# Kernel optimization log

Hardware: AMD Instinct MI355X
Metric: run time of the kernel (lower is better)

Reference implementation:

```python
import jax, jax.numpy as jnp
import numpy as np
from jax import lax

THRESHOLD = 0.3  # nn.Threshold(threshold, 0): y = x if x > threshold else 0
KERNEL = 3       # 3x3 maxpool, stride 1, pad 1 (SAME)


def setup_inputs() -> dict:
    key = jax.random.key(0)
    # [B=1, C=7, H, W] raw feature map (pre-sigmoid logits) from the UNet head
    feature = jax.random.normal(key, (1, 7, 2048, 2048), dtype=jnp.float32)
    return {"feature": feature, "max_detections": 4096}


def reference(feature, max_detections):
    # split along channel dim: 5 keypoint heatmaps, 1 side logit, 1 size logit
    heatmap = feature[:, :5]   # [1,5,H,W]
    side = feature[:, 5:6]     # [1,1,H,W]
    sizes = feature[:, 6:7]    # [1,1,H,W]

    activated = jax.nn.sigmoid(heatmap)
    thresholded = jnp.where(activated > THRESHOLD, activated, jnp.zeros((), activated.dtype))
    # 3x3 stride-1 SAME maxpool (local-max NMS)
    pooled = lax.reduce_window(thresholded, -jnp.inf, lax.max,
                               (1, 1, KERNEL, KERNEL), (1, 1, 1, 1), 'SAME')
    peak_mask = (pooled == thresholded)
    masked = (thresholded * peak_mask.astype(thresholded.dtype))[0]  # [5,H,W]
    masked_bool = masked > 0                                          # [5,H,W]

    side_act = jax.nn.sigmoid(side)[0, 0]    # [H,W]
    sizes_act = jax.nn.sigmoid(sizes)[0, 0]  # [H,W]
    probs_full = jnp.max(activated[0], axis=0)  # [H,W] max over 5 channels

    # fixed-size nonzero (jit-shapeable equivalent of torch .nonzero()/masked_select;
    # entries past the true count are padded with index 0 and zeroed out)
    c, y, x = jnp.nonzero(masked_bool, size=max_detections, fill_value=0)
    n_valid = jnp.sum(masked_bool)
    valid = (jnp.arange(max_detections) < n_valid).astype(probs_full.dtype)

    coords = jnp.stack([c, y, x], axis=1)           # [K,3] like torch nonzero order
    probs = probs_full[y, x] * valid                # masked_select broadcasts [H,W] vs [5,H,W]
    size_width = sizes_act[y, x] * valid
    size_height = sizes_act[y, x] * valid
    side_sel = side_act[y, x] * valid
    return probs, coords, size_width, size_height, side_sel
```

## Files before the change

kernel.cpp:

```cpp
#include <hip/hip_runtime.h>
#include <stdint.h>

#define IMG_H 2048
#define IMG_W 2048
#define CH_PIX (IMG_H * IMG_W)
#define ROWS_PER_BLOCK 8
#define MAXDET 4096
#define NBLK_A 1280
#define WORDS_PER_BLOCK 256

__device__ __forceinline__ float sigmoidf_(float v) {
    return 1.0f / (1.0f + expf(-v));
}

__device__ __forceinline__ float thr_load(const float* __restrict__ chan, int y, int x) {
    if ((unsigned)y >= (unsigned)IMG_H) return 0.0f;
    float a = sigmoidf_(chan[y * IMG_W + x]);
    return a > 0.3f ? a : 0.0f;
}

__global__ __launch_bounds__(256) void zero_out_k(float* __restrict__ out, int n) {
    int i = blockIdx.x * 256 + threadIdx.x;
    if (i < n) out[i] = 0.0f;
}

__global__ __launch_bounds__(256) void pass_a(const float* __restrict__ feat,
                                              uint64_t* __restrict__ masks,
                                              unsigned* __restrict__ counts) {
    int blk = blockIdx.x;
    int c = blk >> 8;
    int ytile = blk & 255;
    int y0 = ytile * ROWS_PER_BLOCK;
    const float* chan = feat + (size_t)c * CH_PIX;
    int t = threadIdx.x;
    int wave = t >> 6, lane = t & 63;

    __shared__ float colmax[IMG_W + 2];
    __shared__ unsigned wsum_lds[4];

    float thrprev[8], thrcur[8], thrnext[8];
#pragma unroll
    for (int j = 0; j < 8; ++j) {
        int x = j * 256 + t;
        thrprev[j] = thr_load(chan, y0 - 1, x);
        thrcur[j]  = thr_load(chan, y0,     x);
    }
    if (t == 0) { colmax[0] = 0.0f; colmax[IMG_W + 1] = 0.0f; }

    unsigned wcnt = 0;
    uint64_t base_widx = (uint64_t)blk * WORDS_PER_BLOCK;

    for (int r = 0; r < ROWS_PER_BLOCK; ++r) {
        int y = y0 + r;
#pragma unroll
        for (int j = 0; j < 8; ++j) {
            int x = j * 256 + t;
            thrnext[j] = thr_load(chan, y + 1, x);
            colmax[x + 1] = fmaxf(fmaxf(thrprev[j], thrcur[j]), thrnext[j]);
        }
        __syncthreads();
#pragma unroll
        for (int j = 0; j < 8; ++j) {
            int x = j * 256 + t;
            float pooled = fmaxf(fmaxf(colmax[x], colmax[x + 1]), colmax[x + 2]);
            bool pred = (thrcur[j] > 0.0f) && (pooled == thrcur[j]);
            uint64_t m = __ballot(pred);
            if (lane == 0) {
                masks[base_widx + (uint64_t)((r * 8 + j) * 4 + wave)] = m;
                wcnt += (unsigned)__popcll(m);
            }
        }
        __syncthreads();
#pragma unroll
        for (int j = 0; j < 8; ++j) { thrprev[j] = thrcur[j]; thrcur[j] = thrnext[j]; }
    }
    if (lane == 0) wsum_lds[wave] = wcnt;
    __syncthreads();
    if (t == 0) counts[blk] = wsum_lds[0] + wsum_lds[1] + wsum_lds[2] + wsum_lds[3];
}

__global__ __launch_bounds__(256) void scan_k(unsigned* __restrict__ data, int n) {
    __shared__ unsigned tmp[256];
    __shared__ unsigned carry;
    int t = threadIdx.x;
    if (t == 0) carry = 0;
    __syncthreads();
    for (int base = 0; base < n; base += 256) {
        unsigned v = (base + t < n) ? data[base + t] : 0u;
        tmp[t] = v;
        __syncthreads();
        for (int off = 1; off < 256; off <<= 1) {
            unsigned u = (t >= off) ? tmp[t - off] : 0u;
            __syncthreads();
            tmp[t] += u;
            __syncthreads();
        }
        unsigned incl = tmp[t];
        unsigned c0 = carry;
        __syncthreads();
        if (base + t < n) data[base + t] = c0 + incl - v;
        if (t == 255) carry = c0 + incl;
        __syncthreads();
    }
}

__global__ __launch_bounds__(256) void pass_c(const float* __restrict__ feat,
                                              const uint64_t* __restrict__ masks,
                                              const unsigned* __restrict__ offsets,
                                              float* __restrict__ out) {
    int blk = blockIdx.x;
    unsigned boff = offsets[blk];
    if (boff >= MAXDET) return;
    int t = threadIdx.x;
    uint64_t w = masks[(uint64_t)blk * WORDS_PER_BLOCK + t];
    unsigned cnt = (unsigned)__popcll(w);
    __shared__ unsigned tmp[256];
    tmp[t] = cnt;
    __syncthreads();
    for (int off = 1; off < 256; off <<= 1) {
        unsigned u = (t >= off) ? tmp[t - off] : 0u;
        __syncthreads();
        tmp[t] += u;
        __syncthreads();
    }
    unsigned rank = boff + tmp[t] - cnt;
    while (w) {
        int b = __ffsll((unsigned long long)w) - 1;
        w &= w - 1;
        if (rank < MAXDET) {
            uint64_t p = ((uint64_t)blk * WORDS_PER_BLOCK + (uint64_t)t) * 64ull + (uint64_t)b;
            int c = (int)(p / CH_PIX);
            int rem = (int)(p % CH_PIX);
            int y = rem >> 11, x = rem & 2047;
            size_t pix = (size_t)y * IMG_W + x;
            float pm = sigmoidf_(feat[pix]);
#pragma unroll
            for (int ch = 1; ch < 5; ++ch)
                pm = fmaxf(pm, sigmoidf_(feat[(size_t)ch * CH_PIX + pix]));
            float sdv = sigmoidf_(feat[(size_t)5 * CH_PIX + pix]);
            float szv = sigmoidf_(feat[(size_t)6 * CH_PIX + pix]);
            out[rank] = pm;
            out[MAXDET + rank * 3 + 0] = (float)c;
            out[MAXDET + rank * 3 + 1] = (float)y;
            out[MAXDET + rank * 3 + 2] = (float)x;
            out[16384 + rank] = szv;
            out[20480 + rank] = szv;
            out[24576 + rank] = sdv;
        }
        rank++;
    }
}

extern "C" void kernel_launch(void* const* d_in, const int* in_sizes, int n_in,
                              void* d_out, int out_size, void* d_ws, size_t ws_size,
                              hipStream_t stream) {
    const float* feat = (const float*)d_in[0];
    float* out = (float*)d_out;
    uint64_t* masks = (uint64_t*)d_ws;
    unsigned* counts = (unsigned*)((char*)d_ws + (size_t)NBLK_A * WORDS_PER_BLOCK * 8);

    zero_out_k<<<(out_size + 255) / 256, 256, 0, stream>>>(out, out_size);
    pass_a<<<NBLK_A, 256, 0, stream>>>(feat, masks, counts);
    scan_k<<<1, 256, 0, stream>>>(counts, NBLK_A);
    pass_c<<<NBLK_A, 256, 0, stream>>>(feat, masks, counts, out);
}
```

Before: 207.0 us.

## Use per-thread 8-pixel strips with byte masks and fold scan into compaction pass

Pass A now gives each thread 8 contiguous pixels loaded as float4s plus halo, computes the 3x3 max in registers, and writes one mask byte per thread per row. This removes the shared-memory colmax and block barriers and doubles rows per block. The separate zero-fill and single-block scan kernels are removed: each compaction block reduces all block counts itself, and the last block zero-fills the tail. Two launches replace four, at the cost of redundant count reductions in every block and halo loads repeated by neighbouring threads.

```diff
diff --git a/kernel.cpp b/kernel.cpp
--- a/kernel.cpp
+++ b/kernel.cpp
@@ -4,116 +4,153 @@
 #define IMG_H 2048
 #define IMG_W 2048
 #define CH_PIX (IMG_H * IMG_W)
-#define ROWS_PER_BLOCK 8
 #define MAXDET 4096
-#define NBLK_A 1280
-#define WORDS_PER_BLOCK 256
+#define NCH_HM 5
+#define ROWS_PER_BLOCK 16
+#define NBLK 640
+#define WPB 512
 
 __device__ __forceinline__ float sigmoidf_(float v) {
     return 1.0f / (1.0f + expf(-v));
 }
-
-__device__ __forceinline__ float thr_load(const float* __restrict__ chan, int y, int x) {
-    if ((unsigned)y >= (unsigned)IMG_H) return 0.0f;
-    float a = sigmoidf_(chan[y * IMG_W + x]);
+__device__ __forceinline__ float sigthr_(float v) {
+    float a = 1.0f / (1.0f + expf(-v));
     return a > 0.3f ? a : 0.0f;
 }
 
-__global__ __launch_bounds__(256) void zero_out_k(float* __restrict__ out, int n) {
-    int i = blockIdx.x * 256 + threadIdx.x;
-    if (i < n) out[i] = 0.0f;
+__device__ __forceinline__ void load_row(const float* __restrict__ chan, int y,
+                                         int xb, float* L) {
+    if ((unsigned)y >= (unsigned)IMG_H) {
+#pragma unroll
+        for (int k = 0; k < 10; ++k) L[k] = 0.0f;
+        return;
+    }
+    const float* row = chan + (size_t)y * IMG_W + xb;
+    float4 a = *(const float4*)(row);
+    float4 b = *(const float4*)(row + 4);
+    L[1] = sigthr_(a.x); L[2] = sigthr_(a.y); L[3] = sigthr_(a.z); L[4] = sigthr_(a.w);
+    L[5] = sigthr_(b.x); L[6] = sigthr_(b.y); L[7] = sigthr_(b.z); L[8] = sigthr_(b.w);
+    L[0] = (xb > 0)            ? sigthr_(row[-1]) : 0.0f;
+    L[9] = (xb + 8 < IMG_W)    ? sigthr_(row[8])  : 0.0f;
 }
 
 __global__ __launch_bounds__(256) void pass_a(const float* __restrict__ feat,
-                                              uint64_t* __restrict__ masks,
+                                              uint8_t* __restrict__ mask_bytes,
                                               unsigned* __restrict__ counts) {
     int blk = blockIdx.x;
-    int c = blk >> 8;
-    int ytile = blk & 255;
-    int y0 = ytile * ROWS_PER_BLOCK;
+    int c = blk >> 7;
+    int ytile = blk & 127;
+    int y0 = ytile << 4;
     const float* chan = feat + (size_t)c * CH_PIX;
     int t = threadIdx.x;
-    int wave = t >> 6, lane = t & 63;
+    int xb = t << 3;
 
-    __shared__ float colmax[IMG_W + 2];
-    __shared__ unsigned wsum_lds[4];
-
-    float thrprev[8], thrcur[8], thrnext[8];
-#pragma unroll
-    for (int j = 0; j < 8; ++j) {
-        int x = j * 256 + t;
-        thrprev[j] = thr_load(chan, y0 - 1, x);
-        thrcur[j]  = thr_load(chan, y0,     x);
-    }
-    if (t == 0) { colmax[0] = 0.0f; colmax[IMG_W + 1] = 0.0f; }
+    float tp[10], tc[10], tn[10];
+    load_row(chan, y0 - 1, xb, tp);
+    load_row(chan, y0,     xb, tc);
 
     unsigned wcnt = 0;
-    uint64_t base_widx = (uint64_t)blk * WORDS_PER_BLOCK;
+    size_t byte_base = (size_t)c * (CH_PIX / 8) + (size_t)y0 * (IMG_W / 8) + t;
 
     for (int r = 0; r < ROWS_PER_BLOCK; ++r) {
-        int y = y0 + r;
+        load_row(chan, y0 + r + 1, xb, tn);
+        float cm[10];
+#pragma unroll
+        for (int k = 0; k < 10; ++k) cm[k] = fmaxf(fmaxf(tp[k], tc[k]), tn[k]);
+        unsigned byte = 0;
 #pragma unroll
         for (int j = 0; j < 8; ++j) {
-            int x = j * 256 + t;
-            thrnext[j] = thr_load(chan, y + 1, x);
-            colmax[x + 1] = fmaxf(fmaxf(thrprev[j], thrcur[j]), thrnext[j]);
+            float own = tc[j + 1];
+            float pooled = fmaxf(fmaxf(cm[j], cm[j + 1]), cm[j + 2]);
+            if (own > 0.0f && pooled == own) byte |= (1u << j);
         }
-        __syncthreads();
+        mask_bytes[byte_base + (size_t)r * (IMG_W / 8)] = (uint8_t)byte;
+        wcnt += __popc(byte);
 #pragma unroll
-        for (int j = 0; j < 8; ++j) {
-            int x = j * 256 + t;
-            float pooled = fmaxf(fmaxf(colmax[x], colmax[x + 1]), colmax[x + 2]);
-            bool pred = (thrcur[j] > 0.0f) && (pooled == thrcur[j]);
-            uint64_t m = __ballot(pred);
-            if (lane == 0) {
-                masks[base_widx + (uint64_t)((r * 8 + j) * 4 + wave)] = m;
-                wcnt += (unsigned)__popcll(m);
-            }
-        }
-        __syncthreads();
+        for (int k = 0; k < 10; ++k) { tp[k] = tc[k]; tc[k] = tn[k]; }
+    }
+
 #pragma unroll
-        for (int j = 0; j < 8; ++j) { thrprev[j] = thrcur[j]; thrcur[j] = thrnext[j]; }
-    }
-    if (lane == 0) wsum_lds[wave] = wcnt;
+    for (int off = 32; off; off >>= 1) wcnt += __shfl_down(wcnt, off, 64);
+    __shared__ unsigned s[4];
+    int wave = t >> 6, lane = t & 63;
+    if (lane == 0) s[wave] = wcnt;
     __syncthreads();
-    if (t == 0) counts[blk] = wsum_lds[0] + wsum_lds[1] + wsum_lds[2] + wsum_lds[3];
+    if (t == 0) counts[blk] = s[0] + s[1] + s[2] + s[3];
 }
 
-__global__ __launch_bounds__(256) void scan_k(unsigned* __restrict__ data, int n) {
-    __shared__ unsigned tmp[256];
-    __shared__ unsigned carry;
-    int t = threadIdx.x;
-    if (t == 0) carry = 0;
-    __syncthreads();
-    for (int base = 0; base < n; base += 256) {
-        unsigned v = (base + t < n) ? data[base + t] : 0u;
-        tmp[t] = v;
-        __syncthreads();
-        for (int off = 1; off < 256; off <<= 1) {
-            unsigned u = (t >= off) ? tmp[t - off] : 0u;
-            __syncthreads();
-            tmp[t] += u;
-            __syncthreads();
+__device__ __forceinline__ void emit_word(uint64_t w, uint64_t pbase, unsigned& rank,
+                                          const float* __restrict__ feat,
+                                          float* __restrict__ out) {
+    while (w) {
+        int b = __ffsll((unsigned long long)w) - 1;
+        w &= w - 1;
+        if (rank < MAXDET) {
+            uint64_t p = pbase + (uint64_t)b;
+            int c = (int)(p >> 22);
+            int rem = (int)(p & (CH_PIX - 1));
+            int y = rem >> 11, x = rem & 2047;
+            size_t pix = (size_t)y * IMG_W + x;
+            float pm = sigmoidf_(feat[pix]);
+#pragma unroll
+            for (int ch = 1; ch < NCH_HM; ++ch)
+                pm = fmaxf(pm, sigmoidf_(feat[(size_t)ch * CH_PIX + pix]));
+            float sdv = sigmoidf_(feat[(size_t)5 * CH_PIX + pix]);
+            float szv = sigmoidf_(feat[(size_t)6 * CH_PIX + pix]);
+            out[rank] = pm;
+            out[MAXDET + rank * 3 + 0] = (float)c;
+            out[MAXDET + rank * 3 + 1] = (float)y;
+            out[MAXDET + rank * 3 + 2] = (float)x;
+            out[4 * MAXDET + rank] = szv;
+            out[5 * MAXDET + rank] = szv;
+            out[6 * MAXDET + rank] = sdv;
         }
-        unsigned incl = tmp[t];
-        unsigned c0 = carry;
-        __syncthreads();
-        if (base + t < n) data[base + t] = c0 + incl - v;
-        if (t == 255) carry = c0 + incl;
-        __syncthreads();
+        rank++;
     }
 }
 
 __global__ __launch_bounds__(256) void pass_c(const float* __restrict__ feat,
                                               const uint64_t* __restrict__ masks,
-                                              const unsigned* __restrict__ offsets,
+                                              const unsigned* __restrict__ counts,
                                               float* __restrict__ out) {
     int blk = blockIdx.x;
-    unsigned boff = offsets[blk];
+    int t = threadIdx.x;
+
+    unsigned p_lt = 0, p_all = 0;
+    for (int i = t; i < NBLK; i += 256) {
+        unsigned v = counts[i];
+        p_all += v;
+        if (i < blk) p_lt += v;
+    }
+#pragma unroll
+    for (int off = 32; off; off >>= 1) {
+        p_lt  += __shfl_down(p_lt,  off, 64);
+        p_all += __shfl_down(p_all, off, 64);
+    }
+    __shared__ unsigned sl[4], sa[4];
+    int wave = t >> 6, lane = t & 63;
+    if (lane == 0) { sl[wave] = p_lt; sa[wave] = p_all; }
+    __syncthreads();
+    unsigned boff  = sl[0] + sl[1] + sl[2] + sl[3];
+    unsigned total = sa[0] + sa[1] + sa[2] + sa[3];
+
+    if (blk == NBLK - 1) {
+        unsigned start = total < MAXDET ? total : MAXDET;
+        for (unsigned k = start + t; k < MAXDET; k += 256) {
+            out[k] = 0.0f;
+            out[MAXDET + 3 * k + 0] = 0.0f;
+            out[MAXDET + 3 * k + 1] = 0.0f;
+            out[MAXDET + 3 * k + 2] = 0.0f;
+            out[4 * MAXDET + k] = 0.0f;
+            out[5 * MAXDET + k] = 0.0f;
+            out[6 * MAXDET + k] = 0.0f;
+        }
+    }
     if (boff >= MAXDET) return;
-    int t = threadIdx.x;
-    uint64_t w = masks[(uint64_t)blk * WORDS_PER_BLOCK + t];
-    unsigned cnt = (unsigned)__popcll(w);
+
+    uint64_t w0 = masks[(size_t)blk * WPB + 2 * t];
+    uint64_t w1 = masks[(size_t)blk * WPB + 2 * t + 1];
+    unsigned cnt = (unsigned)__popcll(w0) + (unsigned)__popcll(w1);
     __shared__ unsigned tmp[256];
     tmp[t] = cnt;
     __syncthreads();
@@ -124,31 +161,9 @@
         __syncthreads();
     }
     unsigned rank = boff + tmp[t] - cnt;
-    while (w) {
-        int b = __ffsll((unsigned long long)w) - 1;
-        w &= w - 1;
-        if (rank < MAXDET) {
-            uint64_t p = ((uint64_t)blk * WORDS_PER_BLOCK + (uint64_t)t) * 64ull + (uint64_t)b;
-            int c = (int)(p / CH_PIX);
-            int rem = (int)(p % CH_PIX);
-            int y = rem >> 11, x = rem & 2047;
-            size_t pix = (size_t)y * IMG_W + x;
-            float pm = sigmoidf_(feat[pix]);
-#pragma unroll
-            for (int ch = 1; ch < 5; ++ch)
-                pm = fmaxf(pm, sigmoidf_(feat[(size_t)ch * CH_PIX + pix]));
-            float sdv = sigmoidf_(feat[(size_t)5 * CH_PIX + pix]);
-            float szv = sigmoidf_(feat[(size_t)6 * CH_PIX + pix]);
-            out[rank] = pm;
-            out[MAXDET + rank * 3 + 0] = (float)c;
-            out[MAXDET + rank * 3 + 1] = (float)y;
-            out[MAXDET + rank * 3 + 2] = (float)x;
-            out[16384 + rank] = szv;
-            out[20480 + rank] = szv;
-            out[24576 + rank] = sdv;
-        }
-        rank++;
-    }
+    uint64_t pbase = (uint64_t)blk * 32768ull + (uint64_t)t * 128ull;
+    emit_word(w0, pbase,      rank, feat, out);
+    emit_word(w1, pbase + 64, rank, feat, out);
 }
 
 extern "C" void kernel_launch(void* const* d_in, const int* in_sizes, int n_in,
@@ -156,11 +171,9 @@
                               hipStream_t stream) {
     const float* feat = (const float*)d_in[0];
     float* out = (float*)d_out;
-    uint64_t* masks = (uint64_t*)d_ws;
-    unsigned* counts = (unsigned*)((char*)d_ws + (size_t)NBLK_A * WORDS_PER_BLOCK * 8);
+    uint8_t* mask_bytes = (uint8_t*)d_ws;
+    unsigned* counts = (unsigned*)((char*)d_ws + (size_t)NBLK * WPB * 8);
 
-    zero_out_k<<<(out_size + 255) / 256, 256, 0, stream>>>(out, out_size);
-    pass_a<<<NBLK_A, 256, 0, stream>>>(feat, masks, counts);
-    scan_k<<<1, 256, 0, stream>>>(counts, NBLK_A);
-    pass_c<<<NBLK_A, 256, 0, stream>>>(feat, masks, counts, out);
+    pass_a<<<NBLK, 256, 0, stream>>>(feat, mask_bytes, counts);
+    pass_c<<<NBLK, 256, 0, stream>>>(feat, (const uint64_t*)mask_bytes, counts, out);
 }
```

After: 238.5 us. +15.2%, slower.
